# Performance work log

Hardware: AMD Instinct MI355X
Metric: run time of the kernel (lower is better)

The kernel has to match this reference:

```python
import jax, jax.numpy as jnp
import numpy as np

EPS = 1e-5
T = 8          # n_segment
PATCH = 3      # corr_size


def _bn(x, g, b):
    # eval-mode BatchNorm with running_mean=0, running_var=1 (init values)
    shape = (1, -1) + (1,) * (x.ndim - 2)
    inv = 1.0 / jnp.sqrt(1.0 + EPS)
    return x * (g * inv).reshape(shape) + b.reshape(shape)


def setup_inputs() -> dict:
    key = jax.random.key(0)
    k1, k2, k3 = jax.random.split(key, 3)
    nt, c, h, w = 64, 256, 56, 56
    cr = 64  # c // reduction, reduction = 4
    return {
        "x": jax.random.normal(k1, (nt, c, h, w), dtype=jnp.float32),
        "conv21_w": jax.random.normal(k2, (cr, c), dtype=jnp.float32) * 0.05,
        "bn21_g": jnp.ones((cr,), jnp.float32),
        "bn21_b": jnp.zeros((cr,), jnp.float32),
        "bn22_g": jnp.ones((PATCH * PATCH,), jnp.float32),
        "bn22_b": jnp.zeros((PATCH * PATCH,), jnp.float32),
        "conv22_w": jax.random.normal(k3, (c, PATCH * PATCH), dtype=jnp.float32) * 0.05,
        "bn23_g": jnp.ones((c,), jnp.float32),
        "bn23_b": jnp.zeros((c,), jnp.float32),
    }


def reference(x, conv21_w, bn21_g, bn21_b, bn22_g, bn22_b, conv22_w, bn23_g, bn23_b):
    nt, c, h, w = x.shape
    n = nt // T
    cr = conv21_w.shape[0]
    residual = x

    # (n, c, T, h, w)
    xv = x.reshape(n, T, c, h, w).transpose(0, 2, 1, 3, 4)
    # conv21: 1x1x1 Conv3d c -> cr, no bias
    y = jnp.einsum('oc,ncthw->nothw', conv21_w, xv)
    y = jax.nn.relu(_bn(y, bn21_g, bn21_b))

    # temporally shifted copy: frame t paired with frame min(t+1, T-1)
    idx = jnp.minimum(jnp.arange(1, T + 1), T - 1)
    y2 = y[:, :, idx, :, :]

    # flatten back to (nt, cr, h, w)
    x1 = y.transpose(0, 2, 1, 3, 4).reshape(nt, cr, h, w)
    x2 = y2.transpose(0, 2, 1, 3, 4).reshape(nt, cr, h, w)

    # SpatialCorrelationSampler(kernel_size=1, patch_size=3): zero-padded
    # displacements (dy, dx) in {-1,0,1}^2, dot product over channels.
    pad = PATCH // 2
    x2p = jnp.pad(x2, ((0, 0), (0, 0), (pad, pad), (pad, pad)))
    cv = jnp.stack(
        [jnp.einsum('nchw,nchw->nhw', x1, x2p[:, :, dy:dy + h, dx:dx + w])
         for dy in range(PATCH) for dx in range(PATCH)],
        axis=1,
    ) / cr  # (nt, 9, h, w), divided by c // (reduction * corr_group)

    cv = jax.nn.relu(_bn(cv, bn22_g, bn22_b))
    # conv22: 1x1 Conv2d 9 -> c, no bias
    out = jnp.einsum('ok,nkhw->nohw', conv22_w, cv)
    out = _bn(out, bn23_g, bn23_b) + residual
    return jax.nn.relu(out)
```

## Files before the change

kernel.cpp:

```cpp
#include <hip/hip_runtime.h>
#include <hip/hip_bf16.h>

#define HW     3136
#define WIDTH  56
#define C      256
#define CR     64
#define NT     64
#define TT     8
#define PW     64
#define PH     58
#define YPLANE (PH*PW)

#define BN_INV 0.9999950000374997f

typedef __attribute__((ext_vector_type(8))) short short8;
typedef __attribute__((ext_vector_type(8))) unsigned short ushort8;
typedef __attribute__((ext_vector_type(4))) float f32x4;
typedef __attribute__((ext_vector_type(2))) float f32x2;
typedef __attribute__((ext_vector_type(4))) unsigned int uint4v;

static __device__ __forceinline__ float relu(float v) { return fmaxf(v, 0.0f); }
static __device__ __forceinline__ float bf2f(unsigned short u) {
    return __builtin_bit_cast(float, (unsigned)u << 16);
}
static __device__ __forceinline__ unsigned short f2bf(float f) {
    unsigned u = __builtin_bit_cast(unsigned, f);
    unsigned r = (u + 0x7FFFu + ((u >> 16) & 1u)) >> 16;
    return (unsigned short)r;
}
static __device__ __forceinline__ unsigned pack2(float a, float b) {
    return (unsigned)f2bf(a) | ((unsigned)f2bf(b) << 16);
}

__global__ __launch_bounds__(256) void k_init(const float* __restrict__ w,
                                              unsigned short* __restrict__ wbf,
                                              uint4v* __restrict__ yz) {
    int blk = blockIdx.x, tid = threadIdx.x;
    if (blk < 1856) {
        size_t b = (size_t)blk * 1024 + tid;
        uint4v z = (uint4v)0u;
        yz[b] = z; yz[b + 256] = z; yz[b + 512] = z; yz[b + 768] = z;
    } else {
        int i = (blk - 1856) * 256 + tid;
        wbf[i] = f2bf(w[i]);
    }
}

__global__ __launch_bounds__(256, 2) void k1_mfma(const float* __restrict__ x,
                                                  const unsigned short* __restrict__ wbf,
                                                  const float* __restrict__ g,
                                                  const float* __restrict__ bb,
                                                  unsigned short* __restrict__ y) {
    __shared__ unsigned short Alds[64][264];
    __shared__ unsigned short Blds[4][64][40];

    const int tid  = threadIdx.x;
    const int lane = tid & 63;
    const int wv   = tid >> 6;
    const int blk  = blockIdx.x;
    const int gq   = blk / 49;
    const int s    = blk - gq * 49;
    const int p0   = s * 64;
    const int nt   = __builtin_amdgcn_readfirstlane(gq * 4 + wv);

    {
        const int o  = tid >> 2;
        const int cb = (tid & 3) * 64;
        const unsigned short* wp = wbf + o * C + cb;
        unsigned short* ap = &Alds[o][cb];
#pragma unroll
        for (int j = 0; j < 8; ++j)
            *(short8*)(ap + j * 8) = *(const short8*)(wp + j * 8);
    }
    __syncthreads();

    const float* xw = x + (size_t)nt * (C * HW) + p0 + lane;
    unsigned short (*Bw)[40] = Blds[wv];

    f32x4 acc[4][4];
#pragma unroll
    for (int nb = 0; nb < 4; ++nb)
#pragma unroll
        for (int mb = 0; mb < 4; ++mb) acc[nb][mb] = (f32x4)0.0f;

    const int frow = lane & 15;
    const int fk8  = (lane >> 4) * 8;

    float buf[2][32];
#pragma unroll
    for (int j = 0; j < 32; ++j) buf[0][j] = xw[(size_t)j * HW];

#pragma unroll
    for (int ks = 0; ks < 8; ++ks) {
        const int cur = ks & 1;
        if (ks < 7) {
            const float* xn = xw + (size_t)((ks + 1) * 32) * HW;
#pragma unroll
            for (int j = 0; j < 32; ++j) buf[cur ^ 1][j] = xn[(size_t)j * HW];
        }
#pragma unroll
        for (int q = 0; q < 4; ++q) {
            union { unsigned d[4]; short8 v; } pk;
#pragma unroll
            for (int jj = 0; jj < 4; ++jj)
                pk.d[jj] = pack2(buf[cur][q * 8 + 2 * jj], buf[cur][q * 8 + 2 * jj + 1]);
            *(short8*)&Bw[lane][q * 8] = pk.v;
        }
        short8 bfrag[4], afrag[4];
#pragma unroll
        for (int nb = 0; nb < 4; ++nb)
            bfrag[nb] = *(const short8*)&Bw[nb * 16 + frow][fk8];
#pragma unroll
        for (int mb = 0; mb < 4; ++mb)
            afrag[mb] = *(const short8*)&Alds[mb * 16 + frow][ks * 32 + fk8];
#pragma unroll
        for (int nb = 0; nb < 4; ++nb)
#pragma unroll
            for (int mb = 0; mb < 4; ++mb)
                acc[nb][mb] = __builtin_amdgcn_mfma_f32_16x16x32_bf16(
                    afrag[mb], bfrag[nb], acc[nb][mb], 0, 0, 0);
    }

    unsigned short* ybase = y + (size_t)nt * CR * YPLANE;
    const int rbase = (lane >> 4) * 4;
#pragma unroll
    for (int nb = 0; nb < 4; ++nb) {
        const int p = p0 + nb * 16 + frow;
        const int r = p / WIDTH;
        const int c = p - r * WIDTH;
        const int pidx = (r + 1) * PW + (c + 1);
#pragma unroll
        for (int mb = 0; mb < 4; ++mb)
#pragma unroll
            for (int rr = 0; rr < 4; ++rr) {
                int o = mb * 16 + rbase + rr;
                float v = relu(fmaf(acc[nb][mb][rr], g[o] * BN_INV, bb[o]));
                ybase[(size_t)o * YPLANE + pidx] = f2bf(v);
            }
    }
}

__global__ __launch_bounds__(256) void k2_corr(const unsigned short* __restrict__ y,
                                               const float* __restrict__ g,
                                               const float* __restrict__ bb,
                                               float* __restrict__ cv) {
    int gt   = blockIdx.x * 256 + threadIdx.x;
    int h    = gt & 3;
    int task = gt >> 2;
    int nt   = task / 392;
    int rm   = task - nt * 392;
    int r    = rm / 7;
    int cg   = rm - r * 7;
    int c0   = cg * 8;
    int nt2  = ((nt & (TT - 1)) < TT - 1) ? nt + 1 : nt;

    const unsigned short* y1 = y + ((size_t)nt * CR + h * 16) * YPLANE
                                 + (size_t)(r + 1) * PW + c0;
    const unsigned short* y2 = y + ((size_t)nt2 * CR + h * 16) * YPLANE
                                 + (size_t)r * PW + c0;

    float acc[9][8];
#pragma unroll
    for (int k = 0; k < 9; ++k)
#pragma unroll
        for (int px = 0; px < 8; ++px) acc[k][px] = 0.0f;

#pragma unroll 2
    for (int ch = 0; ch < 16; ++ch) {
        const unsigned short* p1 = y1 + (size_t)ch * YPLANE;
        ushort8 a8 = *(const ushort8*)p1;
        unsigned at = *(const unsigned*)(p1 + 8);
        float a[8];
#pragma unroll
        for (int j = 0; j < 7; ++j) a[j] = bf2f(a8[j + 1]);
        a[7] = bf2f((unsigned short)(at & 0xffffu));

        const unsigned short* p2 = y2 + (size_t)ch * YPLANE;
#pragma unroll
        for (int dy = 0; dy < 3; ++dy) {
            const unsigned short* pr = p2 + dy * PW;
            ushort8 b8 = *(const ushort8*)pr;
            unsigned bt = *(const unsigned*)(pr + 8);
            float w[10];
#pragma unroll
            for (int j = 0; j < 8; ++j) w[j] = bf2f(b8[j]);
            w[8] = bf2f((unsigned short)(bt & 0xffffu));
            w[9] = bf2f((unsigned short)(bt >> 16));
#pragma unroll
            for (int dx = 0; dx < 3; ++dx) {
                int k = dy * 3 + dx;
#pragma unroll
                for (int px = 0; px < 8; ++px)
                    acc[k][px] = fmaf(a[px], w[px + dx], acc[k][px]);
            }
        }
    }

#pragma unroll
    for (int k = 0; k < 9; ++k)
#pragma unroll
        for (int px = 0; px < 8; ++px) {
            float v = acc[k][px];
            v += __shfl_xor(v, 1);
            v += __shfl_xor(v, 2);
            acc[k][px] = v;
        }

    if (h == 0) {
        float* cp = cv + (size_t)nt * 9 * HW + r * WIDTH + c0;
        const float rcr = 1.0f / CR;
#pragma unroll
        for (int k = 0; k < 9; ++k) {
            float sc = g[k] * BN_INV, bv = bb[k];
            f32x4 lo, hi;
            lo.x = relu(fmaf(acc[k][0] * rcr, sc, bv));
            lo.y = relu(fmaf(acc[k][1] * rcr, sc, bv));
            lo.z = relu(fmaf(acc[k][2] * rcr, sc, bv));
            lo.w = relu(fmaf(acc[k][3] * rcr, sc, bv));
            hi.x = relu(fmaf(acc[k][4] * rcr, sc, bv));
            hi.y = relu(fmaf(acc[k][5] * rcr, sc, bv));
            hi.z = relu(fmaf(acc[k][6] * rcr, sc, bv));
            hi.w = relu(fmaf(acc[k][7] * rcr, sc, bv));
            *(f32x4*)(cp + (size_t)k * HW)     = lo;
            *(f32x4*)(cp + (size_t)k * HW + 4) = hi;
        }
    }
}

__global__ __launch_bounds__(256) void k3_conv22(const float* __restrict__ cv,
                                                 const float* __restrict__ w2,
                                                 const float* __restrict__ g,
                                                 const float* __restrict__ bb,
                                                 const float* __restrict__ x,
                                                 float* __restrict__ out) {
    int gt = blockIdx.x * 256 + threadIdx.x;
    int nt = gt / 1568;
    int p2 = (gt - nt * 1568) * 2;

    const float* cp = cv + (size_t)nt * 9 * HW + p2;
    float cvx[9], cvy[9];
#pragma unroll
    for (int k = 0; k < 9; ++k) {
        f32x2 v = *(const f32x2*)(cp + (size_t)k * HW);
        cvx[k] = v.x; cvy[k] = v.y;
    }

    const float* xp = x   + (size_t)nt * (C * HW) + p2;
    float*       op = out + (size_t)nt * (C * HW) + p2;

#pragma unroll 8
    for (int o = 0; o < C; ++o) {
        const float* wr = w2 + o * 9;
        f32x2 xr = *(const f32x2*)(xp + (size_t)o * HW);
        float sx = 0.0f, sy = 0.0f;
#pragma unroll
        for (int k = 0; k < 9; ++k) {
            float wv = wr[k];
            sx = fmaf(wv, cvx[k], sx);
            sy = fmaf(wv, cvy[k], sy);
        }
        float sc = g[o] * BN_INV, bv = bb[o];
        f32x2 rv;
        rv.x = relu(fmaf(sx, sc, bv) + xr.x);
        rv.y = relu(fmaf(sy, sc, bv) + xr.y);
        *(f32x2*)(op + (size_t)o * HW) = rv;
    }
}

extern "C" void kernel_launch(void* const* d_in, const int* in_sizes, int n_in,
                              void* d_out, int out_size, void* d_ws, size_t ws_size,
                              hipStream_t stream) {
    const float* x   = (const float*)d_in[0];
    const float* w21 = (const float*)d_in[1];
    const float* g21 = (const float*)d_in[2];
    const float* b21 = (const float*)d_in[3];
    const float* g22 = (const float*)d_in[4];
    const float* b22 = (const float*)d_in[5];
    const float* w22 = (const float*)d_in[6];
    const float* g23 = (const float*)d_in[7];
    const float* b23 = (const float*)d_in[8];
    float* out = (float*)d_out;

    unsigned short* yb = (unsigned short*)d_out;
    float* cvb = (float*)d_ws;
    unsigned short* wbf = (unsigned short*)(cvb + (size_t)NT * 9 * HW);

    k_init   <<<1920, 256, 0, stream>>>(w21, wbf, (uint4v*)yb);
    k1_mfma  <<<784,  256, 0, stream>>>(x, wbf, g21, b21, yb);
    k2_corr  <<<392,  256, 0, stream>>>(yb, g22, b22, cvb);
    k3_conv22<<<392,  256, 0, stream>>>(cvb, w22, g23, b23, x, out);
}
```

Baseline: 175.6 us.

## Fuse correlation with conv22 epilogue and fold init into conv21 kernel

Drops the separate init kernel. Conv21 weights are now converted to bf16 inside the MFMA kernel, and extra blocks of that kernel zero only the halo borders of the padded y planes instead of clearing the whole buffer. When the workspace is large enough, y is kept in the workspace and a new fused kernel computes the 3x3 correlation with 8 lanes per task, then applies the BN, the conv22 projection and the residual ReLU directly, so the intermediate cv tensor never goes to memory. Launch count and global traffic drop, but the fused kernel carries 72 accumulators per thread and must reread x in chunks. The halo-only zeroing relies on k1 fully overwriting the interior.

```diff
diff --git a/kernel.cpp b/kernel.cpp
--- a/kernel.cpp
+++ b/kernel.cpp
@@ -1,5 +1,4 @@
 #include <hip/hip_runtime.h>
-#include <hip/hip_bf16.h>
 
 #define HW     3136
 #define WIDTH  56
@@ -10,6 +9,7 @@
 #define PW     64
 #define PH     58
 #define YPLANE (PH*PW)
+#define YBYTES ((size_t)NT * CR * YPLANE * 2)
 
 #define BN_INV 0.9999950000374997f
 
@@ -17,7 +17,6 @@
 typedef __attribute__((ext_vector_type(8))) unsigned short ushort8;
 typedef __attribute__((ext_vector_type(4))) float f32x4;
 typedef __attribute__((ext_vector_type(2))) float f32x2;
-typedef __attribute__((ext_vector_type(4))) unsigned int uint4v;
 
 static __device__ __forceinline__ float relu(float v) { return fmaxf(v, 0.0f); }
 static __device__ __forceinline__ float bf2f(unsigned short u) {
@@ -32,32 +31,49 @@
     return (unsigned)f2bf(a) | ((unsigned)f2bf(b) << 16);
 }
 
-__global__ __launch_bounds__(256) void k_init(const float* __restrict__ w,
-                                              unsigned short* __restrict__ wbf,
-                                              uint4v* __restrict__ yz) {
-    int blk = blockIdx.x, tid = threadIdx.x;
-    if (blk < 1856) {
-        size_t b = (size_t)blk * 1024 + tid;
-        uint4v z = (uint4v)0u;
-        yz[b] = z; yz[b + 256] = z; yz[b + 512] = z; yz[b + 768] = z;
+static __device__ __forceinline__ void halo_zero(int nt, int tid,
+                                                 unsigned short* __restrict__ y) {
+    const int ch = tid >> 2, part = tid & 3;
+    unsigned short* pl = y + ((size_t)nt * CR + ch) * YPLANE;
+    if (part == 0) {
+        ushort8 z = (ushort8)0;
+#pragma unroll
+        for (int j = 0; j < 8; ++j) *(ushort8*)(pl + j * 8) = z;
+    } else if (part == 1) {
+        ushort8 z = (ushort8)0;
+        unsigned short* q = pl + 57 * PW;
+#pragma unroll
+        for (int j = 0; j < 8; ++j) *(ushort8*)(q + j * 8) = z;
+    } else if (part == 2) {
+        for (int r = 1; r <= 28; ++r) {
+            unsigned short* q = pl + r * PW + 57;
+#pragma unroll
+            for (int j = 0; j < 8; ++j) q[j] = 0;
+        }
     } else {
-        int i = (blk - 1856) * 256 + tid;
-        wbf[i] = f2bf(w[i]);
+        for (int r = 29; r <= 56; ++r) {
+            unsigned short* q = pl + r * PW + 57;
+#pragma unroll
+            for (int j = 0; j < 8; ++j) q[j] = 0;
+        }
+        pl[PW] = 0;
     }
 }
 
 __global__ __launch_bounds__(256, 2) void k1_mfma(const float* __restrict__ x,
-                                                  const unsigned short* __restrict__ wbf,
+                                                  const float* __restrict__ w21,
                                                   const float* __restrict__ g,
                                                   const float* __restrict__ bb,
                                                   unsigned short* __restrict__ y) {
+    const int blk = blockIdx.x;
+    const int tid = threadIdx.x;
+    if (blk >= 784) { halo_zero(blk - 784, tid, y); return; }
+
     __shared__ unsigned short Alds[64][264];
     __shared__ unsigned short Blds[4][64][40];
 
-    const int tid  = threadIdx.x;
     const int lane = tid & 63;
     const int wv   = tid >> 6;
-    const int blk  = blockIdx.x;
     const int gq   = blk / 49;
     const int s    = blk - gq * 49;
     const int p0   = s * 64;
@@ -66,11 +82,17 @@
     {
         const int o  = tid >> 2;
         const int cb = (tid & 3) * 64;
-        const unsigned short* wp = wbf + o * C + cb;
+        const float* wp = w21 + o * C + cb;
         unsigned short* ap = &Alds[o][cb];
 #pragma unroll
-        for (int j = 0; j < 8; ++j)
-            *(short8*)(ap + j * 8) = *(const short8*)(wp + j * 8);
+        for (int j = 0; j < 8; ++j) {
+            f32x4 lo = *(const f32x4*)(wp + j * 8);
+            f32x4 hi = *(const f32x4*)(wp + j * 8 + 4);
+            union { unsigned d[4]; short8 v; } pk;
+            pk.d[0] = pack2(lo.x, lo.y); pk.d[1] = pack2(lo.z, lo.w);
+            pk.d[2] = pack2(hi.x, hi.y); pk.d[3] = pack2(hi.z, hi.w);
+            *(short8*)(ap + j * 8) = pk.v;
+        }
     }
     __syncthreads();
 
@@ -137,6 +159,128 @@
                 float v = relu(fmaf(acc[nb][mb][rr], g[o] * BN_INV, bb[o]));
                 ybase[(size_t)o * YPLANE + pidx] = f2bf(v);
             }
+    }
+}
+
+__global__ __launch_bounds__(256, 3) void k2_fused(const unsigned short* __restrict__ y,
+                                                   const float* __restrict__ g22,
+                                                   const float* __restrict__ b22,
+                                                   const float* __restrict__ w2,
+                                                   const float* __restrict__ g23,
+                                                   const float* __restrict__ b23,
+                                                   const float* __restrict__ x,
+                                                   float* __restrict__ out) {
+    __shared__ float w2s[9][256];
+    __shared__ float b23s[256];
+    {
+        const int o = threadIdx.x;
+        const float sc = g23[o] * BN_INV;
+#pragma unroll
+        for (int k = 0; k < 9; ++k) w2s[k][o] = w2[o * 9 + k] * sc;
+        b23s[o] = b23[o];
+    }
+    __syncthreads();
+
+    const int gt   = blockIdx.x * 256 + threadIdx.x;
+    const int h    = gt & 7;
+    const int task = gt >> 3;
+    const int nt   = task / 392;
+    const int rm   = task - nt * 392;
+    const int r    = rm / 7;
+    const int cg   = rm - r * 7;
+    const int c0   = cg * 8;
+    const int nt2  = ((nt & (TT - 1)) < TT - 1) ? nt + 1 : nt;
+
+    const unsigned short* y1 = y + ((size_t)nt * CR + h * 8) * YPLANE
+                                 + (size_t)(r + 1) * PW + c0;
+    const unsigned short* y2 = y + ((size_t)nt2 * CR + h * 8) * YPLANE
+                                 + (size_t)r * PW + c0;
+
+    float acc[9][8];
+#pragma unroll
+    for (int k = 0; k < 9; ++k)
+#pragma unroll
+        for (int px = 0; px < 8; ++px) acc[k][px] = 0.0f;
+
+#pragma unroll
+    for (int ch = 0; ch < 8; ++ch) {
+        const unsigned short* p1 = y1 + (size_t)ch * YPLANE;
+        ushort8 a8 = *(const ushort8*)p1;
+        unsigned at = *(const unsigned*)(p1 + 8);
+        float a[8];
+#pragma unroll
+        for (int j = 0; j < 7; ++j) a[j] = bf2f(a8[j + 1]);
+        a[7] = bf2f((unsigned short)(at & 0xffffu));
+
+        const unsigned short* p2 = y2 + (size_t)ch * YPLANE;
+#pragma unroll
+        for (int dy = 0; dy < 3; ++dy) {
+            const unsigned short* pr = p2 + dy * PW;
+            ushort8 b8 = *(const ushort8*)pr;
+            unsigned bt = *(const unsigned*)(pr + 8);
+            float w[10];
+#pragma unroll
+            for (int j = 0; j < 8; ++j) w[j] = bf2f(b8[j]);
+            w[8] = bf2f((unsigned short)(bt & 0xffffu));
+            w[9] = bf2f((unsigned short)(bt >> 16));
+#pragma unroll
+            for (int dx = 0; dx < 3; ++dx) {
+                int k = dy * 3 + dx;
+#pragma unroll
+                for (int px = 0; px < 8; ++px)
+                    acc[k][px] = fmaf(a[px], w[px + dx], acc[k][px]);
+            }
+        }
+    }
+
+#pragma unroll
+    for (int k = 0; k < 9; ++k)
+#pragma unroll
+        for (int px = 0; px < 8; ++px) {
+            float v = acc[k][px];
+            v += __shfl_xor(v, 1);
+            v += __shfl_xor(v, 2);
+            v += __shfl_xor(v, 4);
+            acc[k][px] = v;
+        }
+
+#pragma unroll
+    for (int k = 0; k < 9; ++k) {
+        float sck = g22[k] * (BN_INV / (float)CR);
+        float bvk = b22[k];
+#pragma unroll
+        for (int px = 0; px < 8; ++px)
+            acc[k][px] = relu(fmaf(acc[k][px], sck, bvk));
+    }
+
+    const int pxl = rm * 8;
+    const float* xb = x   + (size_t)nt * (C * HW) + pxl;
+    float*       ob = out + (size_t)nt * (C * HW) + pxl;
+
+#pragma unroll 2
+    for (int oi = 0; oi < 32; ++oi) {
+        const int o = h * 32 + oi;
+        float wk[9];
+#pragma unroll
+        for (int k = 0; k < 9; ++k) wk[k] = w2s[k][o];
+        const float bv = b23s[o];
+        f32x4 xlo = *(const f32x4*)(xb + (size_t)o * HW);
+        f32x4 xhi = *(const f32x4*)(xb + (size_t)o * HW + 4);
+        float sv[8];
+#pragma unroll
+        for (int px = 0; px < 8; ++px) {
+            float sx = 0.0f;
+#pragma unroll
+            for (int k = 0; k < 9; ++k) sx = fmaf(wk[k], acc[k][px], sx);
+            sv[px] = sx + bv;
+        }
+        f32x4 olo, ohi;
+        olo.x = relu(sv[0] + xlo.x); olo.y = relu(sv[1] + xlo.y);
+        olo.z = relu(sv[2] + xlo.z); olo.w = relu(sv[3] + xlo.w);
+        ohi.x = relu(sv[4] + xhi.x); ohi.y = relu(sv[5] + xhi.y);
+        ohi.z = relu(sv[6] + xhi.z); ohi.w = relu(sv[7] + xhi.w);
+        *(f32x4*)(ob + (size_t)o * HW)     = olo;
+        *(f32x4*)(ob + (size_t)o * HW + 4) = ohi;
     }
 }
 
@@ -174,7 +318,6 @@
 #pragma unroll
         for (int j = 0; j < 7; ++j) a[j] = bf2f(a8[j + 1]);
         a[7] = bf2f((unsigned short)(at & 0xffffu));
-
         const unsigned short* p2 = y2 + (size_t)ch * YPLANE;
 #pragma unroll
         for (int dy = 0; dy < 3; ++dy) {
@@ -195,7 +338,6 @@
             }
         }
     }
-
 #pragma unroll
     for (int k = 0; k < 9; ++k)
 #pragma unroll
@@ -205,7 +347,6 @@
             v += __shfl_xor(v, 2);
             acc[k][px] = v;
         }
-
     if (h == 0) {
         float* cp = cv + (size_t)nt * 9 * HW + r * WIDTH + c0;
         const float rcr = 1.0f / CR;
@@ -236,7 +377,6 @@
     int gt = blockIdx.x * 256 + threadIdx.x;
     int nt = gt / 1568;
     int p2 = (gt - nt * 1568) * 2;
-
     const float* cp = cv + (size_t)nt * 9 * HW + p2;
     float cvx[9], cvy[9];
 #pragma unroll
@@ -244,10 +384,8 @@
         f32x2 v = *(const f32x2*)(cp + (size_t)k * HW);
         cvx[k] = v.x; cvy[k] = v.y;
     }
-
     const float* xp = x   + (size_t)nt * (C * HW) + p2;
     float*       op = out + (size_t)nt * (C * HW) + p2;
-
 #pragma unroll 8
     for (int o = 0; o < C; ++o) {
         const float* wr = w2 + o * 9;
@@ -281,12 +419,15 @@
     const float* b23 = (const float*)d_in[8];
     float* out = (float*)d_out;
 
-    unsigned short* yb = (unsigned short*)d_out;
-    float* cvb = (float*)d_ws;
-    unsigned short* wbf = (unsigned short*)(cvb + (size_t)NT * 9 * HW);
-
-    k_init   <<<1920, 256, 0, stream>>>(w21, wbf, (uint4v*)yb);
-    k1_mfma  <<<784,  256, 0, stream>>>(x, wbf, g21, b21, yb);
-    k2_corr  <<<392,  256, 0, stream>>>(yb, g22, b22, cvb);
-    k3_conv22<<<392,  256, 0, stream>>>(cvb, w22, g23, b23, x, out);
-}
+    if (ws_size >= YBYTES) {
+        unsigned short* yb = (unsigned short*)d_ws;
+        k1_mfma <<<848, 256, 0, stream>>>(x, w21, g21, b21, yb);
+        k2_fused<<<784, 256, 0, stream>>>(yb, g22, b22, w22, g23, b23, x, out);
+    } else {
+        unsigned short* yb = (unsigned short*)d_out;
+        float* cvb = (float*)d_ws;
+        k1_mfma  <<<848, 256, 0, stream>>>(x, w21, g21, b21, yb);
+        k2_corr  <<<392, 256, 0, stream>>>(yb, g22, b22, cvb);
+        k3_conv22<<<392, 256, 0, stream>>>(cvb, w22, g23, b23, x, out);
+    }
+}
```

Result: slower. 197.1 us (+12.3%).

## Fold init into conv21 kernel, zero only halos, remap blocks across XCDs

Applied to the files above, without the earlier changes.

Removes the separate init kernel. Before, it zeroed the whole padded y buffer and converted the weights to bf16. Now the conv21 kernel converts fp32 weights to bf16 while staging them into LDS, and 64 extra blocks zero only the halo border of each y plane. The y buffer moves from the output buffer into the workspace. Block indices in all three kernels are permuted so that consecutive work lands on the same XCD (blk&7 mapping), which should improve L2 locality. This saves one launch and a large memset write, at the cost of per-block weight conversion and scattered small halo stores.

```diff
diff --git a/kernel.cpp b/kernel.cpp
--- a/kernel.cpp
+++ b/kernel.cpp
@@ -1,5 +1,4 @@
 #include <hip/hip_runtime.h>
-#include <hip/hip_bf16.h>
 
 #define HW     3136
 #define WIDTH  56
@@ -10,6 +9,7 @@
 #define PW     64
 #define PH     58
 #define YPLANE (PH*PW)
+#define YBYTES ((size_t)NT * CR * YPLANE * 2)
 
 #define BN_INV 0.9999950000374997f
 
@@ -17,7 +17,6 @@
 typedef __attribute__((ext_vector_type(8))) unsigned short ushort8;
 typedef __attribute__((ext_vector_type(4))) float f32x4;
 typedef __attribute__((ext_vector_type(2))) float f32x2;
-typedef __attribute__((ext_vector_type(4))) unsigned int uint4v;
 
 static __device__ __forceinline__ float relu(float v) { return fmaxf(v, 0.0f); }
 static __device__ __forceinline__ float bf2f(unsigned short u) {
@@ -32,45 +31,69 @@
     return (unsigned)f2bf(a) | ((unsigned)f2bf(b) << 16);
 }
 
-__global__ __launch_bounds__(256) void k_init(const float* __restrict__ w,
-                                              unsigned short* __restrict__ wbf,
-                                              uint4v* __restrict__ yz) {
-    int blk = blockIdx.x, tid = threadIdx.x;
-    if (blk < 1856) {
-        size_t b = (size_t)blk * 1024 + tid;
-        uint4v z = (uint4v)0u;
-        yz[b] = z; yz[b + 256] = z; yz[b + 512] = z; yz[b + 768] = z;
+static __device__ __forceinline__ void halo_zero(int nt, int tid,
+                                                 unsigned short* __restrict__ y) {
+    const int ch = tid >> 2, part = tid & 3;
+    unsigned short* pl = y + ((size_t)nt * CR + ch) * YPLANE;
+    if (part == 0) {
+        ushort8 z = (ushort8)0;
+#pragma unroll
+        for (int j = 0; j < 8; ++j) *(ushort8*)(pl + j * 8) = z;
+    } else if (part == 1) {
+        ushort8 z = (ushort8)0;
+        unsigned short* q = pl + 57 * PW;
+#pragma unroll
+        for (int j = 0; j < 8; ++j) *(ushort8*)(q + j * 8) = z;
+    } else if (part == 2) {
+        for (int r = 1; r <= 28; ++r) {
+            unsigned short* q = pl + r * PW + 57;
+#pragma unroll
+            for (int j = 0; j < 8; ++j) q[j] = 0;
+        }
     } else {
-        int i = (blk - 1856) * 256 + tid;
-        wbf[i] = f2bf(w[i]);
+        for (int r = 29; r <= 56; ++r) {
+            unsigned short* q = pl + r * PW + 57;
+#pragma unroll
+            for (int j = 0; j < 8; ++j) q[j] = 0;
+        }
+        pl[PW] = 0;
     }
 }
 
 __global__ __launch_bounds__(256, 2) void k1_mfma(const float* __restrict__ x,
-                                                  const unsigned short* __restrict__ wbf,
+                                                  const float* __restrict__ w21,
                                                   const float* __restrict__ g,
                                                   const float* __restrict__ bb,
                                                   unsigned short* __restrict__ y) {
+    const int blk = blockIdx.x;
+    const int tid = threadIdx.x;
+    if (blk >= 784) { halo_zero(blk - 784, tid, y); return; }
+    const int bs = (blk & 7) * 98 + (blk >> 3);
+
     __shared__ unsigned short Alds[64][264];
     __shared__ unsigned short Blds[4][64][40];
 
-    const int tid  = threadIdx.x;
     const int lane = tid & 63;
     const int wv   = tid >> 6;
-    const int blk  = blockIdx.x;
-    const int gq   = blk / 49;
-    const int s    = blk - gq * 49;
+    const int gq   = bs / 49;
+    const int s    = bs - gq * 49;
     const int p0   = s * 64;
     const int nt   = __builtin_amdgcn_readfirstlane(gq * 4 + wv);
 
     {
         const int o  = tid >> 2;
         const int cb = (tid & 3) * 64;
-        const unsigned short* wp = wbf + o * C + cb;
+        const float* wp = w21 + o * C + cb;
         unsigned short* ap = &Alds[o][cb];
 #pragma unroll
-        for (int j = 0; j < 8; ++j)
-            *(short8*)(ap + j * 8) = *(const short8*)(wp + j * 8);
+        for (int j = 0; j < 8; ++j) {
+            f32x4 lo = *(const f32x4*)(wp + j * 8);
+            f32x4 hi = *(const f32x4*)(wp + j * 8 + 4);
+            union { unsigned d[4]; short8 v; } pk;
+            pk.d[0] = pack2(lo.x, lo.y); pk.d[1] = pack2(lo.z, lo.w);
+            pk.d[2] = pack2(hi.x, hi.y); pk.d[3] = pack2(hi.z, hi.w);
+            *(short8*)(ap + j * 8) = pk.v;
+        }
     }
     __syncthreads();
 
@@ -144,7 +167,8 @@
                                                const float* __restrict__ g,
                                                const float* __restrict__ bb,
                                                float* __restrict__ cv) {
-    int gt   = blockIdx.x * 256 + threadIdx.x;
+    const int bs = (blockIdx.x & 7) * 49 + (blockIdx.x >> 3);
+    int gt   = bs * 256 + threadIdx.x;
     int h    = gt & 3;
     int task = gt >> 2;
     int nt   = task / 392;
@@ -233,7 +257,8 @@
                                                  const float* __restrict__ bb,
                                                  const float* __restrict__ x,
                                                  float* __restrict__ out) {
-    int gt = blockIdx.x * 256 + threadIdx.x;
+    const int bs = (blockIdx.x & 7) * 49 + (blockIdx.x >> 3);
+    int gt = bs * 256 + threadIdx.x;
     int nt = gt / 1568;
     int p2 = (gt - nt * 1568) * 2;
 
@@ -281,12 +306,10 @@
     const float* b23 = (const float*)d_in[8];
     float* out = (float*)d_out;
 
-    unsigned short* yb = (unsigned short*)d_out;
-    float* cvb = (float*)d_ws;
-    unsigned short* wbf = (unsigned short*)(cvb + (size_t)NT * 9 * HW);
-
-    k_init   <<<1920, 256, 0, stream>>>(w21, wbf, (uint4v*)yb);
-    k1_mfma  <<<784,  256, 0, stream>>>(x, wbf, g21, b21, yb);
-    k2_corr  <<<392,  256, 0, stream>>>(yb, g22, b22, cvb);
-    k3_conv22<<<392,  256, 0, stream>>>(cvb, w22, g23, b23, x, out);
-}
+    unsigned short* yb  = (unsigned short*)d_ws;
+    float*          cvb = (float*)((char*)d_ws + YBYTES);
+
+    k1_mfma  <<<848, 256, 0, stream>>>(x, w21, g21, b21, yb);
+    k2_corr  <<<392, 256, 0, stream>>>(yb, g22, b22, cvb);
+    k3_conv22<<<392, 256, 0, stream>>>(cvb, w22, g23, b23, x, out);
+}
```

New measurement: 188.8 us. +7.5%, slower.
